# Kernel optimization log

Hardware: AMD Instinct MI355X
Metric: run time of the kernel (lower is better)

Reference implementation:

```python
import jax, jax.numpy as jnp
import numpy as np

T = 65536      # total tokens (flattened ragged batch)
H = 1024       # hidden size
B = 64         # number of segments (documents)
L = 2          # num_labels
EPS = 1e-12    # electra layer_norm_eps


def setup_inputs() -> dict:
    key = jax.random.key(0)
    k1, k2, k3, k4, k5, k6 = jax.random.split(key, 6)
    # ragged segment ids: sorted random ids in [0, B) covering all segments
    rng = np.random.default_rng(0)
    cuts = np.sort(rng.choice(np.arange(1, T), size=B - 1, replace=False))
    lengths = np.diff(np.concatenate([[0], cuts, [T]]))  # B positive lengths summing to T
    segment_ids = jnp.asarray(np.repeat(np.arange(B), lengths), dtype=jnp.int32)
    return {
        "sequence_attention_embeddings": jax.random.normal(k1, (T, H), dtype=jnp.float32),
        "sequence_embeddings": jax.random.normal(k2, (T, H), dtype=jnp.float32),
        "W_dense": jax.random.normal(k3, (H, H), dtype=jnp.float32) / np.sqrt(H),
        "b_dense": jnp.zeros((H,), dtype=jnp.float32),
        "gamma": jnp.ones((H,), dtype=jnp.float32),
        "beta": jnp.zeros((H,), dtype=jnp.float32),
        "W_out": jax.random.normal(k4, (H, L), dtype=jnp.float32) / np.sqrt(H),
        "b_out": jnp.zeros((L,), dtype=jnp.float32),
        "segment_ids": segment_ids,
    }


def reference(sequence_attention_embeddings, sequence_embeddings, W_dense, b_dense,
              gamma, beta, W_out, b_out, segment_ids):
    # dense projection on flattened tokens [T, H]
    h = sequence_attention_embeddings @ W_dense + b_dense
    # dropout is identity in eval mode
    # residual + LayerNorm
    h = h + sequence_embeddings
    mu = jnp.mean(h, axis=-1, keepdims=True)
    var = jnp.mean(jnp.square(h - mu), axis=-1, keepdims=True)
    h = (h - mu) / jnp.sqrt(var + EPS) * gamma + beta
    # ragged split + per-segment mean == fused segment mean
    sums = jax.ops.segment_sum(h, segment_ids, num_segments=B)          # [B, H]
    counts = jax.ops.segment_sum(jnp.ones((h.shape[0],), h.dtype), segment_ids, num_segments=B)
    agg = sums / counts[:, None]
    # final projection to logits [B, L]
    return agg @ W_out + b_out
```

## Files before the change

### kernel.cpp

```cpp
#include <hip/hip_runtime.h>

#define T_TOK 65536
#define HDIM  1024
#define NSEG  64

typedef _Float16 half8  __attribute__((ext_vector_type(8)));
typedef float    f32x4  __attribute__((ext_vector_type(4)));
typedef float    f32x16 __attribute__((ext_vector_type(16)));

#define WT_OFF   0ull
#define U0_OFF   2097152ull
#define U1_OFF   (U0_OFF + 4096ull)
#define CON_OFF  (U1_OFF + 4096ull)
#define ACC_OFF  (CON_OFF + 64ull)
#define CNT_OFF  (ACC_OFF + 512ull)

__global__ void prep_kernel(const float* __restrict__ gamma, const float* __restrict__ beta,
                            const float* __restrict__ wout, const int* __restrict__ segids,
                            float* __restrict__ u0, float* __restrict__ u1,
                            float* __restrict__ consts, float* __restrict__ segacc,
                            int* __restrict__ counts) {
    __shared__ int   starts[65];
    __shared__ float cacc[4];
    int tid = threadIdx.x;
    if (tid < 128) segacc[tid] = 0.f;
    if (tid < 4)   cacc[tid]   = 0.f;
    if (tid == 0) { starts[0] = 0; starts[64] = T_TOK; }
    __syncthreads();

    float g  = gamma[tid], be = beta[tid];
    float w0 = wout[2 * tid], w1 = wout[2 * tid + 1];
    float a0 = g * w0, a1 = g * w1;
    u0[tid] = a0; u1[tid] = a1;
    float v[4] = {a0, a1, be * w0, be * w1};
#pragma unroll
    for (int q = 0; q < 4; ++q) {
        float x = v[q];
#pragma unroll
        for (int off = 32; off > 0; off >>= 1) x += __shfl_down(x, off, 64);
        if ((tid & 63) == 0) atomicAdd(&cacc[q], x);
    }
    for (int i = tid; i < T_TOK - 1; i += 1024) {
        int s0 = segids[i], s1 = segids[i + 1];
        if (s1 != s0) starts[s1] = i + 1;
    }
    __syncthreads();
    if (tid < 64) counts[tid] = starts[tid + 1] - starts[tid];
    if (tid < 4)  consts[tid] = cacc[tid];
}

__global__ void wconv_kernel(const float* __restrict__ W, _Float16* __restrict__ Wt) {
    __shared__ float tile[64][65];
    int bx = blockIdx.x & 15;
    int by = blockIdx.x >> 4;
    int c0 = bx * 64, k0 = by * 64;
    int t  = threadIdx.x;
    int kk = t >> 6, cc = t & 63;
#pragma unroll
    for (int i = 0; i < 16; ++i) {
        int kl = kk * 16 + i;
        tile[cc][kl] = W[(size_t)(k0 + kl) * HDIM + c0 + cc];
    }
    __syncthreads();
#pragma unroll
    for (int i = 0; i < 16; ++i) {
        int cl = kk * 16 + i;
        Wt[(size_t)(c0 + cl) * HDIM + k0 + cc] = (_Float16)tile[cl][cc];
    }
}

#define A_LDS 33280

__global__ __launch_bounds__(512, 2) void gemm_kernel(
    const float* __restrict__ A, const float* __restrict__ R,
    const float* __restrict__ bdense, const _Float16* __restrict__ Wt,
    const float* __restrict__ u0g, const float* __restrict__ u1g,
    const float* __restrict__ consts, const int* __restrict__ segids,
    float* __restrict__ segacc) {
    __shared__ __align__(16) char smem[A_LDS + 512 + 256];
    int tid  = threadIdx.x;
    int lane = tid & 63, wave = tid >> 6;
    int ln = lane & 31, lh = lane >> 5;
    int rowBase = blockIdx.x * 64;
    int colB    = wave * 128;

    f32x16 acc[2][4];
#pragma unroll
    for (int tr = 0; tr < 2; ++tr)
#pragma unroll
        for (int tc = 0; tc < 4; ++tc)
#pragma unroll
            for (int i = 0; i < 16; ++i) acc[tr][tc][i] = 0.f;

    const _Float16* bq[4];
#pragma unroll
    for (int tc = 0; tc < 4; ++tc)
        bq[tc] = Wt + (size_t)(colB + tc * 32 + ln) * HDIM + lh * 8;

    int mloc0 = tid >> 5;
    int khalf = tid & 31;

    for (int kq = 0; kq < 4; ++kq) {
        __syncthreads();
#pragma unroll
        for (int i = 0; i < 4; ++i) {
            int mloc = mloc0 + i * 16;
            const float* src = A + (size_t)(rowBase + mloc) * HDIM + kq * 256 + khalf * 8;
            f32x4 a0 = *(const f32x4*)src;
            f32x4 a1 = *(const f32x4*)(src + 4);
            half8 s;
            s[0] = (_Float16)a0[0]; s[1] = (_Float16)a0[1];
            s[2] = (_Float16)a0[2]; s[3] = (_Float16)a0[3];
            s[4] = (_Float16)a1[0]; s[5] = (_Float16)a1[1];
            s[6] = (_Float16)a1[2]; s[7] = (_Float16)a1[3];
            *(half8*)(smem + khalf * 1040 + mloc * 16) = s;
        }
        __syncthreads();
#pragma unroll
        for (int ks = 0; ks < 16; ++ks) {
            half8 afr[2], bfr[4];
#pragma unroll
            for (int tr = 0; tr < 2; ++tr)
                afr[tr] = *(const half8*)(smem + (ks * 2 + lh) * 1040 + (tr * 32 + ln) * 16);
#pragma unroll
            for (int tc = 0; tc < 4; ++tc)
                bfr[tc] = *(const half8*)(bq[tc] + kq * 256 + ks * 16);
#pragma unroll
            for (int tr = 0; tr < 2; ++tr)
#pragma unroll
                for (int tc = 0; tc < 4; ++tc)
                    acc[tr][tc] = __builtin_amdgcn_mfma_f32_32x32x16_f16(
                        afr[tr], bfr[tc], acc[tr][tc], 0, 0, 0);
        }
    }

    __syncthreads();
    float* red  = (float*)smem;
#pragma unroll
    for (int i = 0; i < 16; ++i) red[tid + i * 512] = 0.f;
    float* sval = (float*)(smem + A_LDS);
    int*   sseg = (int*)(smem + A_LDS + 512);
    __syncthreads();

    float bv[4], u0v[4], u1v[4];
#pragma unroll
    for (int tc = 0; tc < 4; ++tc) {
        int c = colB + tc * 32 + ln;
        bv[tc] = bdense[c]; u0v[tc] = u0g[c]; u1v[tc] = u1g[c];
    }
#pragma unroll
    for (int tr = 0; tr < 2; ++tr)
#pragma unroll
        for (int reg = 0; reg < 16; ++reg) {
            int rIT   = (reg & 3) + 8 * (reg >> 2) + 4 * lh;
            int row64 = tr * 32 + rIT;
            size_t grow = (size_t)(rowBase + row64);
            float s1 = 0.f, s2 = 0.f, p0 = 0.f, p1 = 0.f;
#pragma unroll
            for (int tc = 0; tc < 4; ++tc) {
                float h = acc[tr][tc][reg] + bv[tc] + R[grow * HDIM + colB + tc * 32 + ln];
                s1 += h; s2 += h * h; p0 += h * u0v[tc]; p1 += h * u1v[tc];
            }
            atomicAdd(&red[row64 * 32 + ln], s1);
            atomicAdd(&red[2048 + row64 * 32 + ln], s2);
            atomicAdd(&red[4096 + row64 * 32 + ln], p0);
            atomicAdd(&red[6144 + row64 * 32 + ln], p1);
        }
    __syncthreads();
    if (tid < 64) {
        float s1 = 0.f, s2 = 0.f, p0 = 0.f, p1 = 0.f;
        for (int c = 0; c < 32; ++c) {
            s1 += red[tid * 32 + c];
            s2 += red[2048 + tid * 32 + c];
            p0 += red[4096 + tid * 32 + c];
            p1 += red[6144 + tid * 32 + c];
        }
        float mu  = s1 * (1.f / 1024.f);
        float var = s2 * (1.f / 1024.f) - mu * mu;
        float rsd = rsqrtf(var + 1e-12f);
        sval[tid * 2]     = rsd * (p0 - mu * consts[0]) + consts[2];
        sval[tid * 2 + 1] = rsd * (p1 - mu * consts[1]) + consts[3];
        sseg[tid] = segids[rowBase + tid];
    }
    __syncthreads();
    if (tid < 64) {
        int s = sseg[tid];
        if (tid == 63 || sseg[tid + 1] != s) {
            float a0 = 0.f, a1 = 0.f;
            int rr = tid;
            while (rr >= 0 && sseg[rr] == s) { a0 += sval[rr * 2]; a1 += sval[rr * 2 + 1]; --rr; }
            atomicAdd(&segacc[s * 2],     a0);
            atomicAdd(&segacc[s * 2 + 1], a1);
        }
    }
}

__global__ void finalize_kernel(const float* __restrict__ segacc, const int* __restrict__ counts,
                                const float* __restrict__ bout, float* __restrict__ out) {
    int t = threadIdx.x;
    if (t < 128) {
        int s = t >> 1, l = t & 1;
        out[t] = segacc[t] / (float)counts[s] + bout[l];
    }
}

extern "C" void kernel_launch(void* const* d_in, const int* in_sizes, int n_in,
                              void* d_out, int out_size, void* d_ws, size_t ws_size,
                              hipStream_t stream) {
    const float* A      = (const float*)d_in[0];
    const float* R      = (const float*)d_in[1];
    const float* Wd     = (const float*)d_in[2];
    const float* bdense = (const float*)d_in[3];
    const float* gamma  = (const float*)d_in[4];
    const float* beta   = (const float*)d_in[5];
    const float* wout   = (const float*)d_in[6];
    const float* bout   = (const float*)d_in[7];
    const int*   segids = (const int*)d_in[8];
    float* out = (float*)d_out;

    char* ws = (char*)d_ws;
    _Float16* Wt  = (_Float16*)(ws + WT_OFF);
    float* u0     = (float*)(ws + U0_OFF);
    float* u1     = (float*)(ws + U1_OFF);
    float* consts = (float*)(ws + CON_OFF);
    float* segacc = (float*)(ws + ACC_OFF);
    int*   counts = (int*)(ws + CNT_OFF);

    prep_kernel<<<1, 1024, 0, stream>>>(gamma, beta, wout, segids, u0, u1, consts, segacc, counts);
    wconv_kernel<<<256, 256, 0, stream>>>(Wd, Wt);
    gemm_kernel<<<1024, 512, 0, stream>>>(A, R, bdense, Wt, u0, u1, consts, segids, segacc);
    finalize_kernel<<<1, 128, 0, stream>>>(segacc, counts, bout, out);
}
```

Baseline: 1.056 ms.

## Tile GEMM 2D with LDS-staged weights and split row reduction across kernels

The GEMM moves from full-width 64-row blocks, where each wave streamed its weight fragments straight from global memory, to 128x128 output tiles. B tiles are now prepacked by wconv and copied into LDS with global_load_lds. Block IDs are remapped across XCDs so neighbouring column tiles share A rows. Because each block now sees only part of a row, per-row LayerNorm partial sums are atomically accumulated into a global buffer, and a new rowfinal kernel finishes the normalization and segment sums. Segment-boundary detection moves from a single-block loop to a parallel kernel. The cost is that A is read and converted eight times, and more global atomics and launches are added.

```diff
diff --git a/kernel.cpp b/kernel.cpp
--- a/kernel.cpp
+++ b/kernel.cpp
@@ -8,24 +8,25 @@
 typedef float    f32x4  __attribute__((ext_vector_type(4)));
 typedef float    f32x16 __attribute__((ext_vector_type(16)));
 
-#define WT_OFF   0ull
-#define U0_OFF   2097152ull
-#define U1_OFF   (U0_OFF + 4096ull)
-#define CON_OFF  (U1_OFF + 4096ull)
-#define ACC_OFF  (CON_OFF + 64ull)
-#define CNT_OFF  (ACC_OFF + 512ull)
+typedef __attribute__((address_space(1))) const void gvoid;
+typedef __attribute__((address_space(3))) void lvoid;
+
+#define WT_OFF     0ull
+#define U0_OFF     2097152ull
+#define U1_OFF     (U0_OFF + 4096ull)
+#define CON_OFF    (U1_OFF + 4096ull)
+#define ACC_OFF    (CON_OFF + 64ull)
+#define STARTS_OFF (ACC_OFF + 512ull)
+#define ROWRED_OFF (STARTS_OFF + 512ull)
 
 __global__ void prep_kernel(const float* __restrict__ gamma, const float* __restrict__ beta,
-                            const float* __restrict__ wout, const int* __restrict__ segids,
+                            const float* __restrict__ wout,
                             float* __restrict__ u0, float* __restrict__ u1,
-                            float* __restrict__ consts, float* __restrict__ segacc,
-                            int* __restrict__ counts) {
-    __shared__ int   starts[65];
+                            float* __restrict__ consts, float* __restrict__ segacc) {
     __shared__ float cacc[4];
     int tid = threadIdx.x;
     if (tid < 128) segacc[tid] = 0.f;
     if (tid < 4)   cacc[tid]   = 0.f;
-    if (tid == 0) { starts[0] = 0; starts[64] = T_TOK; }
     __syncthreads();
 
     float g  = gamma[tid], be = beta[tid];
@@ -40,167 +41,180 @@
         for (int off = 32; off > 0; off >>= 1) x += __shfl_down(x, off, 64);
         if ((tid & 63) == 0) atomicAdd(&cacc[q], x);
     }
-    for (int i = tid; i < T_TOK - 1; i += 1024) {
-        int s0 = segids[i], s1 = segids[i + 1];
-        if (s1 != s0) starts[s1] = i + 1;
-    }
-    __syncthreads();
-    if (tid < 64) counts[tid] = starts[tid + 1] - starts[tid];
-    if (tid < 4)  consts[tid] = cacc[tid];
+    __syncthreads();
+    if (tid < 4) consts[tid] = cacc[tid];
+}
+
+__global__ void bounds_kernel(const int* __restrict__ segids, int* __restrict__ starts,
+                              float* __restrict__ rowred) {
+    int gid = blockIdx.x * 1024 + threadIdx.x;
+    ((f32x4*)rowred)[gid] = (f32x4){0.f, 0.f, 0.f, 0.f};
+    if (gid == 0) { starts[0] = 0; starts[NSEG] = T_TOK; }
+    if (gid < T_TOK - 1) {
+        int s0 = segids[gid], s1 = segids[gid + 1];
+        if (s1 != s0) starts[s1] = gid + 1;
+    }
 }
 
 __global__ void wconv_kernel(const float* __restrict__ W, _Float16* __restrict__ Wt) {
-    __shared__ float tile[64][65];
-    int bx = blockIdx.x & 15;
-    int by = blockIdx.x >> 4;
-    int c0 = bx * 64, k0 = by * 64;
+    int b  = blockIdx.x;
+    int cb = b >> 4, kq = b & 15;
     int t  = threadIdx.x;
-    int kk = t >> 6, cc = t & 63;
-#pragma unroll
-    for (int i = 0; i < 16; ++i) {
-        int kl = kk * 16 + i;
-        tile[cc][kl] = W[(size_t)(k0 + kl) * HDIM + c0 + cc];
-    }
-    __syncthreads();
-#pragma unroll
-    for (int i = 0; i < 16; ++i) {
-        int cl = kk * 16 + i;
-        Wt[(size_t)(c0 + cl) * HDIM + k0 + cc] = (_Float16)tile[cl][cc];
-    }
-}
-
-#define A_LDS 33280
-
-__global__ __launch_bounds__(512, 2) void gemm_kernel(
+    half8* outp = (half8*)Wt + (size_t)b * 1024;
+#pragma unroll
+    for (int i = 0; i < 4; ++i) {
+        int c = t + i * 256;
+        int col = c & 127, kh = c >> 7;
+        const float* src = W + (size_t)(kq * 64 + kh * 8) * HDIM + cb * 128 + col;
+        half8 v;
+#pragma unroll
+        for (int j = 0; j < 8; ++j) v[j] = (_Float16)src[(size_t)j * HDIM];
+        outp[c] = v;
+    }
+}
+
+__global__ __launch_bounds__(256, 3) void gemm_kernel(
     const float* __restrict__ A, const float* __restrict__ R,
     const float* __restrict__ bdense, const _Float16* __restrict__ Wt,
     const float* __restrict__ u0g, const float* __restrict__ u1g,
-    const float* __restrict__ consts, const int* __restrict__ segids,
-    float* __restrict__ segacc) {
-    __shared__ __align__(16) char smem[A_LDS + 512 + 256];
+    float* __restrict__ rowred) {
+    __shared__ __align__(16) char smem[32768];
     int tid  = threadIdx.x;
     int lane = tid & 63, wave = tid >> 6;
     int ln = lane & 31, lh = lane >> 5;
-    int rowBase = blockIdx.x * 64;
-    int colB    = wave * 128;
-
-    f32x16 acc[2][4];
+    int wrow = wave >> 1, wcol = wave & 1;
+
+    int bid  = blockIdx.x;
+    int xcd  = bid & 7, seq = bid >> 3;
+    int vcol = seq & 7;
+    int vrow = (seq >> 3) * 8 + xcd;
+    int rowBase = vrow * 128, colBase = vcol * 128;
+
+    f32x16 acc[2][2];
 #pragma unroll
     for (int tr = 0; tr < 2; ++tr)
 #pragma unroll
-        for (int tc = 0; tc < 4; ++tc)
+        for (int tc = 0; tc < 2; ++tc)
 #pragma unroll
             for (int i = 0; i < 16; ++i) acc[tr][tc][i] = 0.f;
 
-    const _Float16* bq[4];
-#pragma unroll
-    for (int tc = 0; tc < 4; ++tc)
-        bq[tc] = Wt + (size_t)(colB + tc * 32 + ln) * HDIM + lh * 8;
-
-    int mloc0 = tid >> 5;
-    int khalf = tid & 31;
-
-    for (int kq = 0; kq < 4; ++kq) {
+    int srow = tid >> 1, shalf = tid & 1;
+    const float* asrc0 = A + (size_t)(rowBase + srow) * HDIM + shalf * 32;
+    char* aLds = smem;
+    char* bLds = smem + 16384;
+    char* aWr  = aLds + (size_t)(shalf * 4 * 128 + srow) * 16;
+    const char* bsrc0 = (const char*)Wt + (size_t)(vcol * 16) * 16384 + wave * 4096 + lane * 16;
+    char* bdst = bLds + wave * 4096;
+
+    for (int kq = 0; kq < 16; ++kq) {
         __syncthreads();
-#pragma unroll
-        for (int i = 0; i < 4; ++i) {
-            int mloc = mloc0 + i * 16;
-            const float* src = A + (size_t)(rowBase + mloc) * HDIM + kq * 256 + khalf * 8;
-            f32x4 a0 = *(const f32x4*)src;
-            f32x4 a1 = *(const f32x4*)(src + 4);
+        const char* bs = bsrc0 + (size_t)kq * 16384;
+#pragma unroll
+        for (int i = 0; i < 4; ++i)
+            __builtin_amdgcn_global_load_lds((gvoid*)(bs + i * 1024),
+                                             (lvoid*)(bdst + i * 1024), 16, 0, 0);
+        const float* as = asrc0 + kq * 64;
+        f32x4 a[8];
+#pragma unroll
+        for (int i = 0; i < 8; ++i) a[i] = *(const f32x4*)(as + i * 4);
+#pragma unroll
+        for (int j = 0; j < 4; ++j) {
+            f32x4 lo = a[2 * j], hi = a[2 * j + 1];
             half8 s;
-            s[0] = (_Float16)a0[0]; s[1] = (_Float16)a0[1];
-            s[2] = (_Float16)a0[2]; s[3] = (_Float16)a0[3];
-            s[4] = (_Float16)a1[0]; s[5] = (_Float16)a1[1];
-            s[6] = (_Float16)a1[2]; s[7] = (_Float16)a1[3];
-            *(half8*)(smem + khalf * 1040 + mloc * 16) = s;
+            s[0] = (_Float16)lo[0]; s[1] = (_Float16)lo[1];
+            s[2] = (_Float16)lo[2]; s[3] = (_Float16)lo[3];
+            s[4] = (_Float16)hi[0]; s[5] = (_Float16)hi[1];
+            s[6] = (_Float16)hi[2]; s[7] = (_Float16)hi[3];
+            *(half8*)(aWr + j * 2048) = s;
         }
         __syncthreads();
 #pragma unroll
-        for (int ks = 0; ks < 16; ++ks) {
-            half8 afr[2], bfr[4];
+        for (int ks = 0; ks < 4; ++ks) {
+            int kh = ks * 2 + lh;
+            half8 afr[2], bfr[2];
 #pragma unroll
             for (int tr = 0; tr < 2; ++tr)
-                afr[tr] = *(const half8*)(smem + (ks * 2 + lh) * 1040 + (tr * 32 + ln) * 16);
-#pragma unroll
-            for (int tc = 0; tc < 4; ++tc)
-                bfr[tc] = *(const half8*)(bq[tc] + kq * 256 + ks * 16);
+                afr[tr] = *(const half8*)(aLds + (size_t)(kh * 128 + wrow * 64 + tr * 32 + ln) * 16);
+#pragma unroll
+            for (int tc = 0; tc < 2; ++tc)
+                bfr[tc] = *(const half8*)(bLds + (size_t)(kh * 128 + wcol * 64 + tc * 32 + ln) * 16);
 #pragma unroll
             for (int tr = 0; tr < 2; ++tr)
 #pragma unroll
-                for (int tc = 0; tc < 4; ++tc)
+                for (int tc = 0; tc < 2; ++tc)
                     acc[tr][tc] = __builtin_amdgcn_mfma_f32_32x32x16_f16(
                         afr[tr], bfr[tc], acc[tr][tc], 0, 0, 0);
         }
     }
 
     __syncthreads();
-    float* red  = (float*)smem;
-#pragma unroll
-    for (int i = 0; i < 16; ++i) red[tid + i * 512] = 0.f;
-    float* sval = (float*)(smem + A_LDS);
-    int*   sseg = (int*)(smem + A_LDS + 512);
-    __syncthreads();
-
-    float bv[4], u0v[4], u1v[4];
-#pragma unroll
-    for (int tc = 0; tc < 4; ++tc) {
-        int c = colB + tc * 32 + ln;
+    float* red = (float*)smem;
+#pragma unroll
+    for (int i = 0; i < 16; ++i) red[tid + i * 256] = 0.f;
+    __syncthreads();
+
+    float bv[2], u0v[2], u1v[2];
+#pragma unroll
+    for (int tc = 0; tc < 2; ++tc) {
+        int c = colBase + wcol * 64 + tc * 32 + ln;
         bv[tc] = bdense[c]; u0v[tc] = u0g[c]; u1v[tc] = u1g[c];
     }
+    int slot = ln & 7;
 #pragma unroll
     for (int tr = 0; tr < 2; ++tr)
 #pragma unroll
         for (int reg = 0; reg < 16; ++reg) {
-            int rIT   = (reg & 3) + 8 * (reg >> 2) + 4 * lh;
-            int row64 = tr * 32 + rIT;
-            size_t grow = (size_t)(rowBase + row64);
-            float s1 = 0.f, s2 = 0.f, p0 = 0.f, p1 = 0.f;
-#pragma unroll
-            for (int tc = 0; tc < 4; ++tc) {
-                float h = acc[tr][tc][reg] + bv[tc] + R[grow * HDIM + colB + tc * 32 + ln];
-                s1 += h; s2 += h * h; p0 += h * u0v[tc]; p1 += h * u1v[tc];
-            }
-            atomicAdd(&red[row64 * 32 + ln], s1);
-            atomicAdd(&red[2048 + row64 * 32 + ln], s2);
-            atomicAdd(&red[4096 + row64 * 32 + ln], p0);
-            atomicAdd(&red[6144 + row64 * 32 + ln], p1);
+            int rIT  = (reg & 3) + 8 * (reg >> 2) + 4 * lh;
+            int rloc = wrow * 64 + tr * 32 + rIT;
+            size_t grow = (size_t)(rowBase + rloc);
+            const float* rp = R + grow * HDIM + colBase + wcol * 64 + ln;
+            float h0 = acc[tr][0][reg] + bv[0] + rp[0];
+            float h1 = acc[tr][1][reg] + bv[1] + rp[32];
+            atomicAdd(&red[(0 * 128 + rloc) * 8 + slot], h0 + h1);
+            atomicAdd(&red[(1 * 128 + rloc) * 8 + slot], h0 * h0 + h1 * h1);
+            atomicAdd(&red[(2 * 128 + rloc) * 8 + slot], h0 * u0v[0] + h1 * u0v[1]);
+            atomicAdd(&red[(3 * 128 + rloc) * 8 + slot], h0 * u1v[0] + h1 * u1v[1]);
         }
     __syncthreads();
-    if (tid < 64) {
-        float s1 = 0.f, s2 = 0.f, p0 = 0.f, p1 = 0.f;
-        for (int c = 0; c < 32; ++c) {
-            s1 += red[tid * 32 + c];
-            s2 += red[2048 + tid * 32 + c];
-            p0 += red[4096 + tid * 32 + c];
-            p1 += red[6144 + tid * 32 + c];
-        }
-        float mu  = s1 * (1.f / 1024.f);
-        float var = s2 * (1.f / 1024.f) - mu * mu;
-        float rsd = rsqrtf(var + 1e-12f);
-        sval[tid * 2]     = rsd * (p0 - mu * consts[0]) + consts[2];
-        sval[tid * 2 + 1] = rsd * (p1 - mu * consts[1]) + consts[3];
-        sseg[tid] = segids[rowBase + tid];
-    }
-    __syncthreads();
-    if (tid < 64) {
-        int s = sseg[tid];
-        if (tid == 63 || sseg[tid + 1] != s) {
-            float a0 = 0.f, a1 = 0.f;
-            int rr = tid;
-            while (rr >= 0 && sseg[rr] == s) { a0 += sval[rr * 2]; a1 += sval[rr * 2 + 1]; --rr; }
-            atomicAdd(&segacc[s * 2],     a0);
-            atomicAdd(&segacc[s * 2 + 1], a1);
-        }
-    }
-}
-
-__global__ void finalize_kernel(const float* __restrict__ segacc, const int* __restrict__ counts,
+    for (int s = tid; s < 512; s += 256) {
+        int q = s >> 7, row = s & 127;
+        const float* rr = &red[(q * 128 + row) * 8];
+        float v = rr[0] + rr[1] + rr[2] + rr[3] + rr[4] + rr[5] + rr[6] + rr[7];
+        atomicAdd(&rowred[(size_t)(rowBase + row) * 4 + q], v);
+    }
+}
+
+__global__ void rowfinal_kernel(const float* __restrict__ rowred, const int* __restrict__ segids,
+                                const float* __restrict__ consts, float* __restrict__ segacc) {
+    __shared__ float sval[256][2];
+    __shared__ int   sseg[256];
+    int t   = threadIdx.x;
+    int row = blockIdx.x * 256 + t;
+    f32x4 v = ((const f32x4*)rowred)[row];
+    float mu  = v[0] * (1.f / 1024.f);
+    float var = v[1] * (1.f / 1024.f) - mu * mu;
+    float rsd = rsqrtf(var + 1e-12f);
+    sval[t][0] = rsd * (v[2] - mu * consts[0]) + consts[2];
+    sval[t][1] = rsd * (v[3] - mu * consts[1]) + consts[3];
+    sseg[t] = segids[row];
+    __syncthreads();
+    int s = sseg[t];
+    if (t == 255 || sseg[t + 1] != s) {
+        float a0 = 0.f, a1 = 0.f;
+        int rr = t;
+        while (rr >= 0 && sseg[rr] == s) { a0 += sval[rr][0]; a1 += sval[rr][1]; --rr; }
+        atomicAdd(&segacc[s * 2],     a0);
+        atomicAdd(&segacc[s * 2 + 1], a1);
+    }
+}
+
+__global__ void finalize_kernel(const float* __restrict__ segacc, const int* __restrict__ starts,
                                 const float* __restrict__ bout, float* __restrict__ out) {
     int t = threadIdx.x;
     if (t < 128) {
         int s = t >> 1, l = t & 1;
-        out[t] = segacc[t] / (float)counts[s] + bout[l];
+        int cnt = starts[s + 1] - starts[s];
+        out[t] = segacc[t] / (float)cnt + bout[l];
     }
 }
 
@@ -224,10 +238,13 @@
     float* u1     = (float*)(ws + U1_OFF);
     float* consts = (float*)(ws + CON_OFF);
     float* segacc = (float*)(ws + ACC_OFF);
-    int*   counts = (int*)(ws + CNT_OFF);
-
-    prep_kernel<<<1, 1024, 0, stream>>>(gamma, beta, wout, segids, u0, u1, consts, segacc, counts);
-    wconv_kernel<<<256, 256, 0, stream>>>(Wd, Wt);
-    gemm_kernel<<<1024, 512, 0, stream>>>(A, R, bdense, Wt, u0, u1, consts, segids, segacc);
-    finalize_kernel<<<1, 128, 0, stream>>>(segacc, counts, bout, out);
-}
+    int*   starts = (int*)(ws + STARTS_OFF);
+    float* rowred = (float*)(ws + ROWRED_OFF);
+
+    prep_kernel<<<1, 1024, 0, stream>>>(gamma, beta, wout, u0, u1, consts, segacc);
+    bounds_kernel<<<64, 1024, 0, stream>>>(segids, starts, rowred);
+    wconv_kernel<<<128, 256, 0, stream>>>(Wd, Wt);
+    gemm_kernel<<<4096, 256, 0, stream>>>(A, R, bdense, Wt, u0, u1, rowred);
+    rowfinal_kernel<<<256, 256, 0, stream>>>(rowred, segids, consts, segacc);
+    finalize_kernel<<<1, 128, 0, stream>>>(segacc, starts, bout, out);
+}
```

After: 1.350 ms. 27.9% more time.
